# Performance work log

Measured on AMD Instinct MI355X. Metric: run time of the kernel, lower is better.

Reference implementation:

```python
import jax, jax.numpy as jnp
import numpy as np

BN_EPS = 1e-5  # PyTorch BatchNorm1d default eps (Dice's self.eps is unused by its bn)

def _bn(x):
    # training-mode BatchNorm1d without affine: batch mean / biased variance
    m = jnp.mean(x, axis=0)
    v = jnp.var(x, axis=0)
    return (x - m) * jax.lax.rsqrt(v + BN_EPS)

def _dice(x, alpha):
    p = jax.nn.sigmoid(_bn(x))
    return alpha * (1.0 - p) * x + p * x

def setup_inputs():
    key = jax.random.key(0)
    ks = jax.random.split(key, 48)
    B, L = 8192, 200
    Vu, Vd, Va, Vs, Vg, Vt, Vf = 100001, 1001, 50001, 20001, 20001, 501, 100001
    f = jnp.float32
    s = 0.05
    inp = {}
    inp['dense'] = jax.random.normal(ks[0], (B, 16), f)
    inp['userid'] = jax.random.randint(ks[1], (B,), 0, Vu)
    inp['device'] = jax.random.randint(ks[2], (B,), 0, Vd)
    inp['authorid'] = jax.random.randint(ks[3], (B,), 0, Va)
    inp['bgm_song_id'] = jax.random.randint(ks[4], (B,), 0, Vs)
    inp['bgm_singer_id'] = jax.random.randint(ks[5], (B,), 0, Vg)
    inp['manual_tag'] = jax.random.randint(ks[6], (B,), 0, Vt)
    inp['feedid'] = jax.random.randint(ks[7], (B,), 0, Vf)
    inp['seq_ids'] = jax.random.randint(ks[8], (B, L), 0, Vf)
    inp['seq_len'] = jax.random.randint(ks[9], (B,), 1, L + 1)
    # embedding tables (dims hard-coded in the torch module)
    inp['emb_userid'] = s * jax.random.normal(ks[10], (Vu, 16), f)
    inp['emb_device'] = s * jax.random.normal(ks[11], (Vd, 2), f)
    inp['emb_authorid'] = s * jax.random.normal(ks[12], (Va, 4), f)
    inp['emb_song'] = s * jax.random.normal(ks[13], (Vs, 4), f)
    inp['emb_singer'] = s * jax.random.normal(ks[14], (Vg, 4), f)
    inp['emb_tag'] = s * jax.random.normal(ks[15], (Vt, 4), f)
    inp['emb_feedid'] = s * jax.random.normal(ks[16], (Vf, 16), f)
    inp['emb_seq'] = s * jax.random.normal(ks[17], (Vf, 16), f)
    # attention MLP: 4*16 -> 64 -> 32 -> 1
    inp['aW1'] = s * jax.random.normal(ks[18], (64, 64), f)
    inp['ab1'] = jnp.zeros((64,), f)
    inp['aW2'] = s * jax.random.normal(ks[19], (64, 32), f)
    inp['ab2'] = jnp.zeros((32,), f)
    inp['aW3'] = s * jax.random.normal(ks[20], (32, 1), f)
    inp['ab3'] = jnp.zeros((1,), f)
    # FCN stack: 82 -> 512 -> 256 -> 128 -> 1, Dice alpha + affine BN per layer
    dims = [82, 512, 256, 128]
    for i in range(3):
        inp[f'W{i}'] = s * jax.random.normal(ks[21 + i], (dims[i], dims[i + 1]), f)
        inp[f'b{i}'] = jnp.zeros((dims[i + 1],), f)
        inp[f'alpha{i}'] = jnp.zeros((dims[i + 1],), f)
        inp[f'g{i}'] = jnp.ones((dims[i + 1],), f)
        inp[f'beta{i}'] = jnp.zeros((dims[i + 1],), f)
    inp['Wout'] = s * jax.random.normal(ks[30], (128, 1), f)
    inp['bout'] = jnp.zeros((1,), f)
    return inp

def _forward(dense, userid, device, authorid, bgm_song_id, bgm_singer_id, manual_tag,
             feedid, seq_ids, seq_len,
             emb_userid, emb_device, emb_authorid, emb_song, emb_singer, emb_tag,
             emb_feedid, emb_seq,
             aW1, ab1, aW2, ab2, aW3, ab3,
             W0, b0, alpha0, g0, beta0,
             W1, b1, alpha1, g1, beta1,
             W2, b2, alpha2, g2, beta2,
             Wout, bout):
    B, L = seq_ids.shape
    # embedding lookups
    cat_embs = [emb_userid[userid], emb_device[device], emb_authorid[authorid],
                emb_song[bgm_song_id], emb_singer[bgm_singer_id], emb_tag[manual_tag]]
    q = emb_feedid[feedid]            # [B, 16]
    keys = emb_seq[seq_ids]           # [B, L, 16]
    # DIN attention: cross features + 3-layer MLP score
    qe = jnp.broadcast_to(q[:, None, :], keys.shape)
    cross = jnp.concatenate([qe, keys, qe - keys, qe * keys], axis=2)  # [B, L, 64]
    h = jax.nn.relu(cross @ aW1 + ab1)
    h = jax.nn.relu(h @ aW2 + ab2)
    score = (h @ aW3 + ab3)[..., 0]   # [B, L]
    mask = jnp.arange(L)[None, :] < seq_len[:, None]
    w = jnp.where(mask, score, 0.0)   # is_softmax=False branch
    att_out = jnp.sum(w[:, :, None] * keys, axis=1)  # [B, 16]
    # dense MLP stack with Dice + affine BN (dropout is identity at eval)
    net = jnp.concatenate([dense] + cat_embs + [q, att_out], axis=1)  # [B, 82]
    for W, b, a, g, be in ((W0, b0, alpha0, g0, beta0),
                           (W1, b1, alpha1, g1, beta1),
                           (W2, b2, alpha2, g2, beta2)):
        net = net @ W + b
        net = _dice(net, a)
        net = g * _bn(net) + be
    logit = net @ Wout + bout
    prob = jax.nn.sigmoid(logit)
    emb_vars = jnp.concatenate(cat_embs + [q, att_out], axis=1)
    l2_reg = 0.2 * jnp.mean(jnp.linalg.norm(emb_vars, axis=1))
    return prob, logit, l2_reg

def reference(dense, userid, device, authorid, bgm_song_id, bgm_singer_id, manual_tag,
              feedid, seq_ids, seq_len,
              emb_userid, emb_device, emb_authorid, emb_song, emb_singer, emb_tag,
              emb_feedid, emb_seq,
              aW1, ab1, aW2, ab2, aW3, ab3,
              W0, b0, alpha0, g0, beta0,
              W1, b1, alpha1, g1, beta1,
              W2, b2, alpha2, g2, beta2,
              Wout, bout):
    return _forward(dense, userid, device, authorid, bgm_song_id, bgm_singer_id, manual_tag,
                    feedid, seq_ids, seq_len,
                    emb_userid, emb_device, emb_authorid, emb_song, emb_singer, emb_tag,
                    emb_feedid, emb_seq,
                    aW1, ab1, aW2, ab2, aW3, ab3,
                    W0, b0, alpha0, g0, beta0,
                    W1, b1, alpha1, g1, beta1,
                    W2, b2, alpha2, g2, beta2,
                    Wout, bout)
```

## Files before the change

### kernel.cpp

```cpp
#include <hip/hip_runtime.h>
#include <hip/hip_bf16.h>

#define B_ 8192
#define L_ 200

typedef __attribute__((ext_vector_type(4))) short s4v;
typedef __attribute__((ext_vector_type(8))) short s8v;
typedef __attribute__((ext_vector_type(16))) float f32x16;

__device__ __forceinline__ short f2bf(float f) {
    union { float f; unsigned u; } v; v.f = f;
    unsigned r = (v.u + 0x7fffu + ((v.u >> 16) & 1u)) >> 16;
    return (short)r;
}
__device__ __forceinline__ float bf2f(short s) {
    union { unsigned u; float f; } v; v.u = ((unsigned)(unsigned short)s) << 16;
    return v.f;
}
__device__ __forceinline__ unsigned pk2(float a, float b) {
    return ((unsigned)(unsigned short)f2bf(b) << 16) | (unsigned)(unsigned short)f2bf(a);
}

#define OFF_ATT   0
#define OFF_NETBF (OFF_ATT + B_*16)
#define OFF_X     (OFF_NETBF + B_*64)
#define OFF_D0    (OFF_X + B_*512)
#define OFF_D1    (OFF_D0 + B_*256)
#define OFF_D2    (OFF_D1 + B_*128)
#define OFF_ACC   (OFF_D2 + B_*64)
#define OFF_NORM  (OFF_ACC + 12*512)
#define OFF_PREP  (OFF_NORM + 1)
#define OFF_W0T   (OFF_PREP + 4096)
#define OFF_W1T   (OFF_W0T + 32768)
#define OFF_W2T   (OFF_W1T + 65536)
#define OFF_FB1   (OFF_W2T + 16384)
#define OFF_FB2   (OFF_FB1 + 256)

__global__ __launch_bounds__(256) void init_ws(float* acc, float* fb) {
    for (int i = threadIdx.x; i < 12*512 + 1; i += 256) acc[i] = 0.f;
    if (threadIdx.x < 256 + 128) fb[threadIdx.x] = 0.f;
}

__global__ __launch_bounds__(256) void prep_w(
    const float* __restrict__ aW1, const float* __restrict__ aW2,
    const float* __restrict__ W0, float* __restrict__ wsP, short* __restrict__ W0T)
{
    const int t = threadIdx.x;
    if (blockIdx.x == 0) {
        float* W1B = wsP;
        float* W1D = wsP + 1024;
        float* W1AC = wsP + 2048;
        short* W2F = (short*)(wsP + 3072);
        for (int idx = t; idx < 1024; idx += 256) {
            int r = idx & 7, l = (idx >> 3) & 63, mt = idx >> 9;
            int i = ((l >> 5) << 3) + r, j = mt * 32 + (l & 31);
            W1B[idx] = aW1[(16 + i) * 64 + j] - aW1[(32 + i) * 64 + j];
            W1D[idx] = aW1[(48 + i) * 64 + j];
        }
        for (int idx = t; idx < 1024; idx += 256) {
            int i = idx & 15, j = idx >> 4;
            W1AC[idx] = aW1[i * 64 + j] + aW1[(32 + i) * 64 + j];
        }
        for (int idx = t; idx < 2048; idx += 256) {
            int r = idx & 7, l = (idx >> 3) & 63, ks = idx >> 9;
            int j2 = ks * 16 + ((l >> 5) << 3) + r, n2 = l & 31;
            W2F[idx] = f2bf(aW2[j2 * 32 + n2]);
        }
    }
    for (int idx = blockIdx.x * 256 + t; idx < 512 * 128; idx += 32 * 256) {
        int n = idx & 511, k = idx >> 9;
        W0T[n * 128 + k] = (k < 82) ? f2bf(W0[k * 512 + n]) : (short)0;
    }
}

__global__ __launch_bounds__(256) void prep_fold(
    const float* __restrict__ W, const float* __restrict__ bias,
    const float* __restrict__ sD, const float* __restrict__ qD,
    const float* __restrict__ g, const float* __restrict__ be,
    float invB, int K, int N,
    short* __restrict__ WT, float* __restrict__ fb)
{
    __shared__ short tile[64][65];
    __shared__ float sclS[64], sftS[64];
    __shared__ float red[256];
    const int t = threadIdx.x;
    const int bn = blockIdx.x * 64, bk = blockIdx.y * 64;

    if (t < 64) {
        const int k = bk + t;
        float m = sD[k] * invB;
        float v = fmaf(-m, m, qD[k] * invB);
        float sc = g[k] * rsqrtf(v + 1e-5f);
        sclS[t] = sc;
        sftS[t] = be[k] - m * sc;
    }
    __syncthreads();

    const int nn = t & 63, kk0 = (t >> 6) * 16;
    float part = 0.f;
    #pragma unroll
    for (int i = 0; i < 16; ++i) {
        const int kk = kk0 + i;
        float w = W[(size_t)(bk + kk) * N + bn + nn];
        tile[kk][nn] = f2bf(sclS[kk] * w);
        part = fmaf(sftS[kk], w, part);
    }
    red[t] = part;
    __syncthreads();

    {
        const int n = t >> 2, kp = (t & 3) * 16;
        short* dst = &WT[(size_t)(bn + n) * K + bk + kp];
        #pragma unroll
        for (int i = 0; i < 16; ++i) dst[i] = tile[kp + i][n];
    }
    if (t < 64) {
        float s = red[t] + red[t + 64] + red[t + 128] + red[t + 192];
        if (blockIdx.y == 0) s += bias[bn + t];
        atomicAdd(&fb[bn + t], s);
    }
}

__global__ __launch_bounds__(256) void attn_k(
    const int* __restrict__ feedid, const int* __restrict__ seq_ids,
    const int* __restrict__ seq_len,
    const float* __restrict__ e_feed, const float* __restrict__ e_seq,
    const float* __restrict__ ab1, const float* __restrict__ ab2,
    const float* __restrict__ ab3, const float* __restrict__ aW3,
    const float* __restrict__ wsP, float* __restrict__ att)
{
    __shared__ short KL[224 * 20];
    __shared__ float qS[16];
    __shared__ float qtS[64];
    __shared__ float w3S[32], ab2S[32];
    __shared__ float wS[224];
    __shared__ float pS[16 * 16];

    const float* W1B = wsP;
    const float* W1D = wsP + 1024;
    const float* W1AC = wsP + 2048;
    const short* W2F = (const short*)(wsP + 3072);

    const int b = blockIdx.x, t = threadIdx.x;

    if (t < 16) qS[t] = e_feed[(size_t)feedid[b] * 16 + t];
    if (t >= 32 && t < 64) w3S[t - 32] = aW3[t - 32];
    if (t >= 64 && t < 96) ab2S[t - 64] = ab2[t - 64];
    __syncthreads();

    for (int idx = t; idx < 800; idx += 256) {
        int row = idx >> 2, p = idx & 3;
        int sid = seq_ids[(size_t)b * L_ + row];
        const float4 f4 = ((const float4*)(e_seq + (size_t)sid * 16))[p];
        s4v v; v[0] = f2bf(f4.x); v[1] = f2bf(f4.y); v[2] = f2bf(f4.z); v[3] = f2bf(f4.w);
        *(s4v*)&KL[row * 20 + p * 4] = v;
    }
    if (t < 96) {
        s4v z = {0, 0, 0, 0};
        *(s4v*)&KL[(200 + (t >> 2)) * 20 + (t & 3) * 4] = z;
    }
    if (t < 64) {
        float s = ab1[t];
        #pragma unroll
        for (int i = 0; i < 16; ++i) s = fmaf(qS[i], W1AC[t * 16 + i], s);
        qtS[t] = s;
    }
    __syncthreads();

    const int h = (t >> 5) & 1, l31 = t & 31, l63 = t & 63, wv = t >> 6;

    union U8 { s8v s; unsigned u[4]; };

    U8 a1[2];
    #pragma unroll
    for (int mt = 0; mt < 2; ++mt)
        #pragma unroll
        for (int r = 0; r < 8; ++r) {
            int idx = (mt * 64 + l63) * 8 + r;
            float v = fmaf(qS[h * 8 + r], W1D[idx], W1B[idx]);
            a1[mt].s[r] = f2bf(v);
        }
    s8v w2f[4];
    #pragma unroll
    for (int ks = 0; ks < 4; ++ks)
        w2f[ks] = *(const s8v*)&W2F[(ks * 64 + l63) * 8];

    const float ab3v = ab3[0];
    const int len = seq_len[b];

    for (int m = wv; m < 7; m += 4) {
        const int row = m * 32 + l31;
        s8v bK;
        {
            s4v lo = *(const s4v*)&KL[row * 20 + h * 8];
            s4v hi = *(const s4v*)&KL[row * 20 + h * 8 + 4];
            bK[0] = lo[0]; bK[1] = lo[1]; bK[2] = lo[2]; bK[3] = lo[3];
            bK[4] = hi[0]; bK[5] = hi[1]; bK[6] = hi[2]; bK[7] = hi[3];
        }

        f32x16 c2;
        #pragma unroll
        for (int i = 0; i < 16; ++i) c2[i] = 0.f;

        #pragma unroll
        for (int mt = 0; mt < 2; ++mt) {
            f32x16 c;
            #pragma unroll
            for (int i = 0; i < 16; ++i) c[i] = 0.f;
            c = __builtin_amdgcn_mfma_f32_32x32x16_bf16(a1[mt].s, bK, c, 0, 0, 0);

            unsigned pk[8], pks[8];
            #pragma unroll
            for (int i = 0; i < 8; ++i) {
                int r0 = 2 * i, r1 = r0 + 1;
                float v0 = fmaxf(c[r0] + qtS[mt * 32 + (r0 & 3) + 8 * (r0 >> 2) + 4 * h], 0.f);
                float v1 = fmaxf(c[r1] + qtS[mt * 32 + (r1 & 3) + 8 * (r1 >> 2) + 4 * h], 0.f);
                pk[i] = pk2(v0, v1);
                pks[i] = __shfl_xor(pk[i], 32);
            }
            {
                U8 bf2;
                bf2.u[0] = h ? pks[2] : pk[0];
                bf2.u[1] = h ? pks[3] : pk[1];
                bf2.u[2] = h ? pk[2]  : pks[0];
                bf2.u[3] = h ? pk[3]  : pks[1];
                c2 = __builtin_amdgcn_mfma_f32_32x32x16_bf16(w2f[mt * 2], bf2.s, c2, 0, 0, 0);
            }
            {
                U8 bf2;
                bf2.u[0] = h ? pks[6] : pk[4];
                bf2.u[1] = h ? pks[7] : pk[5];
                bf2.u[2] = h ? pk[6]  : pks[4];
                bf2.u[3] = h ? pk[7]  : pks[5];
                c2 = __builtin_amdgcn_mfma_f32_32x32x16_bf16(w2f[mt * 2 + 1], bf2.s, c2, 0, 0, 0);
            }
        }

        float part = 0.f;
        #pragma unroll
        for (int r = 0; r < 16; ++r) {
            int n2 = (r & 3) + 8 * (r >> 2) + 4 * h;
            part = fmaf(fmaxf(c2[r] + ab2S[n2], 0.f), w3S[n2], part);
        }
        float tot = part + __shfl_xor(part, 32) + ab3v;
        if (h == 0) wS[row] = (row < len) ? tot : 0.f;
    }
    __syncthreads();

    {
        const int c = t & 15, ch = t >> 4, r0 = ch * 14;
        float s = 0.f;
        #pragma unroll
        for (int i = 0; i < 14; ++i)
            s = fmaf(wS[r0 + i], bf2f(KL[(r0 + i) * 20 + c]), s);
        pS[ch * 16 + c] = s;
    }
    __syncthreads();
    if (t < 16) {
        float s = 0.f;
        #pragma unroll
        for (int ch = 0; ch < 16; ++ch) s += pS[ch * 16 + t];
        att[(size_t)b * 16 + t] = s;
    }
}

__global__ __launch_bounds__(256) void build_net(
    const float* __restrict__ dense,
    const int* __restrict__ userid, const int* __restrict__ device_,
    const int* __restrict__ authorid, const int* __restrict__ song,
    const int* __restrict__ singer, const int* __restrict__ tag,
    const int* __restrict__ feedid,
    const float* __restrict__ e_user, const float* __restrict__ e_dev,
    const float* __restrict__ e_auth, const float* __restrict__ e_song,
    const float* __restrict__ e_singer, const float* __restrict__ e_tag,
    const float* __restrict__ e_feed,
    const float* __restrict__ att, short* __restrict__ nbf,
    float* __restrict__ norm_acc)
{
    const int b = blockIdx.x * 256 + threadIdx.x;
    float row[82];
    const float* d = dense + (size_t)b * 16;
    #pragma unroll
    for (int i = 0; i < 16; ++i) row[i] = d[i];
    const float* eu = e_user + (size_t)userid[b] * 16;
    #pragma unroll
    for (int i = 0; i < 16; ++i) row[16 + i] = eu[i];
    const float* ed = e_dev + (size_t)device_[b] * 2;
    row[32] = ed[0]; row[33] = ed[1];
    const float* ea = e_auth + (size_t)authorid[b] * 4;
    #pragma unroll
    for (int i = 0; i < 4; ++i) row[34 + i] = ea[i];
    const float* es = e_song + (size_t)song[b] * 4;
    #pragma unroll
    for (int i = 0; i < 4; ++i) row[38 + i] = es[i];
    const float* eg = e_singer + (size_t)singer[b] * 4;
    #pragma unroll
    for (int i = 0; i < 4; ++i) row[42 + i] = eg[i];
    const float* et = e_tag + (size_t)tag[b] * 4;
    #pragma unroll
    for (int i = 0; i < 4; ++i) row[46 + i] = et[i];
    const float* ef = e_feed + (size_t)feedid[b] * 16;
    #pragma unroll
    for (int i = 0; i < 16; ++i) row[50 + i] = ef[i];
    const float* at = att + (size_t)b * 16;
    #pragma unroll
    for (int i = 0; i < 16; ++i) row[66 + i] = at[i];

    float sq = 0.f;
    #pragma unroll
    for (int i = 16; i < 82; ++i) sq = fmaf(row[i], row[i], sq);

    union { unsigned w[64]; uint4 w4[16]; } U;
    #pragma unroll
    for (int i = 0; i < 41; ++i) U.w[i] = pk2(row[2 * i], row[2 * i + 1]);
    #pragma unroll
    for (int i = 41; i < 64; ++i) U.w[i] = 0u;
    uint4* op = (uint4*)(nbf + (size_t)b * 128);
    #pragma unroll
    for (int c = 0; c < 16; ++c) op[c] = U.w4[c];

    float nrm = sqrtf(sq);
    nrm += __shfl_xor(nrm, 32); nrm += __shfl_xor(nrm, 16);
    nrm += __shfl_xor(nrm, 8);  nrm += __shfl_xor(nrm, 4);
    nrm += __shfl_xor(nrm, 2);  nrm += __shfl_xor(nrm, 1);
    if ((threadIdx.x & 63) == 0) atomicAdd(norm_acc, nrm);
}

__global__ __launch_bounds__(256) void gemm_mfma_stats(
    const short* __restrict__ A, int lda,
    const short* __restrict__ BT, int ldb,
    const float* __restrict__ bias,
    float* __restrict__ C, int N, int K,
    float* __restrict__ sout, float* __restrict__ qout)
{
    __shared__ short As[128 * 68];
    __shared__ short Bs[64 * 68];
    __shared__ float colS[64], colQ[64];

    const int bm = blockIdx.y * 128, bn = blockIdx.x * 64;
    const int t = threadIdx.x;
    const int wv = t >> 6, l31 = t & 31, h = (t >> 5) & 1;

    if (t < 64) { colS[t] = 0.f; colQ[t] = 0.f; }

    const int arow0 = t >> 3, apart = (t & 7) * 8;
    s8v ar[4], br[2];

    {   const int k0 = 0;
        #pragma unroll
        for (int i = 0; i < 4; ++i)
            ar[i] = *(const s8v*)&A[(size_t)(bm + arow0 + i * 32) * lda + k0 + apart];
        #pragma unroll
        for (int i = 0; i < 2; ++i)
            br[i] = *(const s8v*)&BT[(size_t)(bn + arow0 + i * 32) * ldb + k0 + apart];
    }

    f32x16 acc0, acc1;
    #pragma unroll
    for (int i = 0; i < 16; ++i) { acc0[i] = 0.f; acc1[i] = 0.f; }

    const int nk = K >> 6;
    for (int kc = 0; kc < nk; ++kc) {
        #pragma unroll
        for (int i = 0; i < 4; ++i)
            *(s8v*)&As[(arow0 + i * 32) * 68 + apart] = ar[i];
        #pragma unroll
        for (int i = 0; i < 2; ++i)
            *(s8v*)&Bs[(arow0 + i * 32) * 68 + apart] = br[i];
        __syncthreads();
        if (kc + 1 < nk) {
            const int k0 = (kc + 1) << 6;
            #pragma unroll
            for (int i = 0; i < 4; ++i)
                ar[i] = *(const s8v*)&A[(size_t)(bm + arow0 + i * 32) * lda + k0 + apart];
            #pragma unroll
            for (int i = 0; i < 2; ++i)
                br[i] = *(const s8v*)&BT[(size_t)(bn + arow0 + i * 32) * ldb + k0 + apart];
        }
        #pragma unroll
        for (int ks = 0; ks < 4; ++ks) {
            const s8v af  = *(const s8v*)&As[(wv * 32 + l31) * 68 + ks * 16 + h * 8];
            const s8v bf0 = *(const s8v*)&Bs[l31 * 68 + ks * 16 + h * 8];
            const s8v bf1 = *(const s8v*)&Bs[(32 + l31) * 68 + ks * 16 + h * 8];
            acc0 = __builtin_amdgcn_mfma_f32_32x32x16_bf16(af, bf0, acc0, 0, 0, 0);
            acc1 = __builtin_amdgcn_mfma_f32_32x32x16_bf16(af, bf1, acc1, 0, 0, 0);
        }
        __syncthreads();
    }

    #pragma unroll
    for (int ns = 0; ns < 2; ++ns) {
        const int col = bn + ns * 32 + l31;
        const float bv = bias[col];
        float s = 0.f, q = 0.f;
        const f32x16& ac = ns ? acc1 : acc0;
        #pragma unroll
        for (int r = 0; r < 16; ++r) {
            const int row = bm + wv * 32 + (r & 3) + 8 * (r >> 2) + 4 * h;
            float x = ac[r] + bv;
            C[(size_t)row * N + col] = x;
            s += x; q = fmaf(x, x, q);
        }
        s += __shfl_xor(s, 32);
        q += __shfl_xor(q, 32);
        if (h == 0) {
            atomicAdd(&colS[ns * 32 + l31], s);
            atomicAdd(&colQ[ns * 32 + l31], q);
        }
    }
    __syncthreads();
    if (t < 64) {
        atomicAdd(&sout[bn + t], colS[t]);
        atomicAdd(&qout[bn + t], colQ[t]);
    }
}

__global__ __launch_bounds__(256) void dice_stats(
    const float* __restrict__ X, short* __restrict__ D,
    const float* __restrict__ sin_, const float* __restrict__ qin_,
    const float* __restrict__ alpha,
    float* __restrict__ sout, float* __restrict__ qout,
    int N, float invB)
{
    __shared__ float cS[64], cQ[64];
    const int t = threadIdx.x;
    const int col = blockIdx.x * 64 + (t & 63);
    const int r0 = blockIdx.y * 64 + (t >> 6);
    if (t < 64) { cS[t] = 0.f; cQ[t] = 0.f; }
    __syncthreads();

    const float m = sin_[col] * invB;
    const float v = fmaf(-m, m, qin_[col] * invB);
    const float rs = rsqrtf(v + 1e-5f);
    const float al = alpha[col];

    float s = 0.f, q = 0.f;
    #pragma unroll
    for (int i = 0; i < 16; ++i) {
        const int r = r0 + i * 4;
        const float x = X[(size_t)r * N + col];
        const float xn = (x - m) * rs;
        const float p = 1.f / (1.f + __expf(-xn));
        const float d = x * (p + al * (1.f - p));
        D[(size_t)r * N + col] = f2bf(d);
        s += d; q = fmaf(d, d, q);
    }
    atomicAdd(&cS[t & 63], s);
    atomicAdd(&cQ[t & 63], q);
    __syncthreads();
    if (t < 64) {
        atomicAdd(&sout[blockIdx.x * 64 + t], cS[t]);
        atomicAdd(&qout[blockIdx.x * 64 + t], cQ[t]);
    }
}

__global__ __launch_bounds__(256) void final_k(
    const short* __restrict__ Y, const float* __restrict__ Wout,
    const float* __restrict__ bout, const float* __restrict__ norm_acc,
    const float* __restrict__ sD, const float* __restrict__ qD,
    const float* __restrict__ g, const float* __restrict__ be,
    float invB, float* __restrict__ out)
{
    const int wv = threadIdx.x >> 6, lane = threadIdx.x & 63;
    const int b = blockIdx.x * 4 + wv;
    const short* y = Y + (size_t)b * 128;

    float s = 0.f;
    #pragma unroll
    for (int hh = 0; hh < 2; ++hh) {
        const int c = hh * 64 + lane;
        const float m = sD[c] * invB;
        const float v = fmaf(-m, m, qD[c] * invB);
        const float yn = g[c] * (bf2f(y[c]) - m) * rsqrtf(v + 1e-5f) + be[c];
        s = fmaf(yn, Wout[c], s);
    }
    s += __shfl_xor(s, 32); s += __shfl_xor(s, 16);
    s += __shfl_xor(s, 8);  s += __shfl_xor(s, 4);
    s += __shfl_xor(s, 2);  s += __shfl_xor(s, 1);
    if (lane == 0) {
        float logit = s + bout[0];
        out[B_ + b] = logit;
        out[b] = 1.f / (1.f + __expf(-logit));
    }
    if (blockIdx.x == 0 && threadIdx.x == 0)
        out[2 * B_] = 0.2f * norm_acc[0] / (float)B_;
}

extern "C" void kernel_launch(void* const* d_in, const int* in_sizes, int n_in,
                              void* d_out, int out_size, void* d_ws, size_t ws_size,
                              hipStream_t stream)
{
    const float* dense    = (const float*)d_in[0];
    const int*   userid   = (const int*)d_in[1];
    const int*   device_  = (const int*)d_in[2];
    const int*   authorid = (const int*)d_in[3];
    const int*   song     = (const int*)d_in[4];
    const int*   singer   = (const int*)d_in[5];
    const int*   tag      = (const int*)d_in[6];
    const int*   feedid   = (const int*)d_in[7];
    const int*   seq_ids  = (const int*)d_in[8];
    const int*   seq_len  = (const int*)d_in[9];
    const float* e_user   = (const float*)d_in[10];
    const float* e_dev    = (const float*)d_in[11];
    const float* e_auth   = (const float*)d_in[12];
    const float* e_song   = (const float*)d_in[13];
    const float* e_singer = (const float*)d_in[14];
    const float* e_tag    = (const float*)d_in[15];
    const float* e_feed   = (const float*)d_in[16];
    const float* e_seq    = (const float*)d_in[17];
    const float* aW1 = (const float*)d_in[18];
    const float* ab1 = (const float*)d_in[19];
    const float* aW2 = (const float*)d_in[20];
    const float* ab2 = (const float*)d_in[21];
    const float* aW3 = (const float*)d_in[22];
    const float* ab3 = (const float*)d_in[23];
    const float* W0 = (const float*)d_in[24]; const float* b0 = (const float*)d_in[25];
    const float* al0 = (const float*)d_in[26]; const float* g0 = (const float*)d_in[27];
    const float* be0 = (const float*)d_in[28];
    const float* W1 = (const float*)d_in[29]; const float* b1 = (const float*)d_in[30];
    const float* al1 = (const float*)d_in[31]; const float* g1 = (const float*)d_in[32];
    const float* be1 = (const float*)d_in[33];
    const float* W2 = (const float*)d_in[34]; const float* b2 = (const float*)d_in[35];
    const float* al2 = (const float*)d_in[36]; const float* g2 = (const float*)d_in[37];
    const float* be2 = (const float*)d_in[38];
    const float* Wout = (const float*)d_in[39]; const float* bout = (const float*)d_in[40];

    float* ws    = (float*)d_ws;
    float* att   = ws + OFF_ATT;
    short* netbf = (short*)(ws + OFF_NETBF);
    float* X     = ws + OFF_X;
    short* d0    = (short*)(ws + OFF_D0);
    short* d1    = (short*)(ws + OFF_D1);
    short* d2    = (short*)(ws + OFF_D2);
    float* acc   = ws + OFF_ACC;
    float* norm  = ws + OFF_NORM;
    float* prep  = ws + OFF_PREP;
    short* W0T   = (short*)(ws + OFF_W0T);
    short* W1T   = (short*)(ws + OFF_W1T);
    short* W2T   = (short*)(ws + OFF_W2T);
    float* fb1   = ws + OFF_FB1;
    float* fb2   = ws + OFF_FB2;
    float* out   = (float*)d_out;

    float* sX0 = acc + 0*512;  float* qX0 = acc + 1*512;
    float* sD0 = acc + 2*512;  float* qD0 = acc + 3*512;
    float* sX1 = acc + 4*512;  float* qX1 = acc + 5*512;
    float* sD1 = acc + 6*512;  float* qD1 = acc + 7*512;
    float* sX2 = acc + 8*512;  float* qX2 = acc + 9*512;
    float* sD2 = acc + 10*512; float* qD2 = acc + 11*512;

    const float invB = 1.f / (float)B_;

    hipLaunchKernelGGL(init_ws, dim3(1), dim3(256), 0, stream, acc, fb1);
    hipLaunchKernelGGL(prep_w, dim3(32), dim3(256), 0, stream, aW1, aW2, W0, prep, W0T);

    hipLaunchKernelGGL(attn_k, dim3(B_), dim3(256), 0, stream,
                       feedid, seq_ids, seq_len, e_feed, e_seq,
                       ab1, ab2, ab3, aW3, prep, att);

    hipLaunchKernelGGL(build_net, dim3(B_/256), dim3(256), 0, stream,
                       dense, userid, device_, authorid, song, singer, tag, feedid,
                       e_user, e_dev, e_auth, e_song, e_singer, e_tag, e_feed,
                       att, netbf, norm);

    hipLaunchKernelGGL(gemm_mfma_stats, dim3(512/64, B_/128), dim3(256), 0, stream,
                       netbf, 128, W0T, 128, b0, X, 512, 128, sX0, qX0);
    hipLaunchKernelGGL(dice_stats, dim3(512/64, B_/64), dim3(256), 0, stream,
                       X, d0, sX0, qX0, al0, sD0, qD0, 512, invB);
    hipLaunchKernelGGL(prep_fold, dim3(256/64, 512/64), dim3(256), 0, stream,
                       W1, b1, sD0, qD0, g0, be0, invB, 512, 256, W1T, fb1);

    hipLaunchKernelGGL(gemm_mfma_stats, dim3(256/64, B_/128), dim3(256), 0, stream,
                       d0, 512, W1T, 512, fb1, X, 256, 512, sX1, qX1);
    hipLaunchKernelGGL(dice_stats, dim3(256/64, B_/64), dim3(256), 0, stream,
                       X, d1, sX1, qX1, al1, sD1, qD1, 256, invB);
    hipLaunchKernelGGL(prep_fold, dim3(128/64, 256/64), dim3(256), 0, stream,
                       W2, b2, sD1, qD1, g1, be1, invB, 256, 128, W2T, fb2);

    hipLaunchKernelGGL(gemm_mfma_stats, dim3(128/64, B_/128), dim3(256), 0, stream,
                       d1, 256, W2T, 256, fb2, X, 128, 256, sX2, qX2);
    hipLaunchKernelGGL(dice_stats, dim3(128/64, B_/64), dim3(256), 0, stream,
                       X, d2, sX2, qX2, al2, sD2, qD2, 128, invB);

    hipLaunchKernelGGL(final_k, dim3(B_/4), dim3(256), 0, stream,
                       d2, Wout, bout, norm, sD2, qD2, g2, be2, invB, out);
}
```

Baseline: 300.9 us.

## Use MFMA for query-dependent attention weights, shrink GEMM tiles, merge init kernel

Several changes at once. The attention kernel no longer builds a per-block query-scaled first-layer weight in registers. It precomputes key*query products in shared memory and issues a second MFMA, with bf16 weight fragments loaded from the prep buffer. The zero-init kernel is folded into prep_w as an extra block, which saves a launch, and float-to-bf16 packing now uses the v_cvt_pk_bf16_f32 instruction. The GEMM tile shrinks from 128x64 to 64x64 with one accumulator per wave, which doubles the grid for more parallelism but gives less reuse per tile.

```diff
diff --git a/kernel.cpp b/kernel.cpp
--- a/kernel.cpp
+++ b/kernel.cpp
@@ -17,8 +17,10 @@
     union { unsigned u; float f; } v; v.u = ((unsigned)(unsigned short)s) << 16;
     return v.f;
 }
-__device__ __forceinline__ unsigned pk2(float a, float b) {
-    return ((unsigned)(unsigned short)f2bf(b) << 16) | (unsigned)(unsigned short)f2bf(a);
+__device__ __forceinline__ unsigned cvtpk(float a, float b) {
+    unsigned r;
+    asm("v_cvt_pk_bf16_f32 %0, %1, %2" : "=v"(r) : "v"(a), "v"(b));
+    return r;
 }
 
 #define OFF_ATT   0
@@ -36,26 +38,22 @@
 #define OFF_FB1   (OFF_W2T + 16384)
 #define OFF_FB2   (OFF_FB1 + 256)
 
-__global__ __launch_bounds__(256) void init_ws(float* acc, float* fb) {
-    for (int i = threadIdx.x; i < 12*512 + 1; i += 256) acc[i] = 0.f;
-    if (threadIdx.x < 256 + 128) fb[threadIdx.x] = 0.f;
-}
-
 __global__ __launch_bounds__(256) void prep_w(
     const float* __restrict__ aW1, const float* __restrict__ aW2,
-    const float* __restrict__ W0, float* __restrict__ wsP, short* __restrict__ W0T)
+    const float* __restrict__ W0, float* __restrict__ wsP, short* __restrict__ W0T,
+    float* __restrict__ acc, float* __restrict__ fb)
 {
     const int t = threadIdx.x;
     if (blockIdx.x == 0) {
-        float* W1B = wsP;
-        float* W1D = wsP + 1024;
-        float* W1AC = wsP + 2048;
-        short* W2F = (short*)(wsP + 3072);
+        short* W1BC = (short*)wsP;
+        short* W1D  = (short*)(wsP + 512);
+        float* W1AC = wsP + 1024;
+        short* W2F  = (short*)(wsP + 2048);
         for (int idx = t; idx < 1024; idx += 256) {
             int r = idx & 7, l = (idx >> 3) & 63, mt = idx >> 9;
             int i = ((l >> 5) << 3) + r, j = mt * 32 + (l & 31);
-            W1B[idx] = aW1[(16 + i) * 64 + j] - aW1[(32 + i) * 64 + j];
-            W1D[idx] = aW1[(48 + i) * 64 + j];
+            W1BC[idx] = f2bf(aW1[(16 + i) * 64 + j] - aW1[(32 + i) * 64 + j]);
+            W1D[idx]  = f2bf(aW1[(48 + i) * 64 + j]);
         }
         for (int idx = t; idx < 1024; idx += 256) {
             int i = idx & 15, j = idx >> 4;
@@ -66,10 +64,14 @@
             int j2 = ks * 16 + ((l >> 5) << 3) + r, n2 = l & 31;
             W2F[idx] = f2bf(aW2[j2 * 32 + n2]);
         }
-    }
-    for (int idx = blockIdx.x * 256 + t; idx < 512 * 128; idx += 32 * 256) {
-        int n = idx & 511, k = idx >> 9;
-        W0T[n * 128 + k] = (k < 82) ? f2bf(W0[k * 512 + n]) : (short)0;
+    } else if (blockIdx.x == 33) {
+        for (int i = t; i < 12 * 512 + 1; i += 256) acc[i] = 0.f;
+        if (t < 256 + 128) fb[t] = 0.f;
+    } else {
+        for (int idx = (blockIdx.x - 1) * 256 + t; idx < 512 * 128; idx += 32 * 256) {
+            int n = idx & 511, k = idx >> 9;
+            W0T[n * 128 + k] = (k < 82) ? f2bf(W0[k * 512 + n]) : (short)0;
+        }
     }
 }
 
@@ -130,34 +132,44 @@
     const float* __restrict__ wsP, float* __restrict__ att)
 {
     __shared__ short KL[224 * 20];
+    __shared__ short KQ[224 * 20];
+    __shared__ int   sidS[224];
     __shared__ float qS[16];
     __shared__ float qtS[64];
     __shared__ float w3S[32], ab2S[32];
     __shared__ float wS[224];
     __shared__ float pS[16 * 16];
 
-    const float* W1B = wsP;
-    const float* W1D = wsP + 1024;
-    const float* W1AC = wsP + 2048;
-    const short* W2F = (const short*)(wsP + 3072);
+    const short* W1BC = (const short*)wsP;
+    const short* W1D  = (const short*)(wsP + 512);
+    const float* W1AC = wsP + 1024;
+    const short* W2F  = (const short*)(wsP + 2048);
 
     const int b = blockIdx.x, t = threadIdx.x;
 
     if (t < 16) qS[t] = e_feed[(size_t)feedid[b] * 16 + t];
     if (t >= 32 && t < 64) w3S[t - 32] = aW3[t - 32];
     if (t >= 64 && t < 96) ab2S[t - 64] = ab2[t - 64];
+    if (t < 200) sidS[t] = seq_ids[(size_t)b * L_ + t];
     __syncthreads();
 
     for (int idx = t; idx < 800; idx += 256) {
-        int row = idx >> 2, p = idx & 3;
-        int sid = seq_ids[(size_t)b * L_ + row];
+        int row = idx >> 2, p = idx & 3, c0 = p * 4;
+        int sid = sidS[row];
         const float4 f4 = ((const float4*)(e_seq + (size_t)sid * 16))[p];
-        s4v v; v[0] = f2bf(f4.x); v[1] = f2bf(f4.y); v[2] = f2bf(f4.z); v[3] = f2bf(f4.w);
-        *(s4v*)&KL[row * 20 + p * 4] = v;
+        uint2 kk, kq;
+        kk.x = cvtpk(f4.x, f4.y);
+        kk.y = cvtpk(f4.z, f4.w);
+        kq.x = cvtpk(f4.x * qS[c0],     f4.y * qS[c0 + 1]);
+        kq.y = cvtpk(f4.z * qS[c0 + 2], f4.w * qS[c0 + 3]);
+        *(uint2*)&KL[row * 20 + c0] = kk;
+        *(uint2*)&KQ[row * 20 + c0] = kq;
     }
     if (t < 96) {
-        s4v z = {0, 0, 0, 0};
-        *(s4v*)&KL[(200 + (t >> 2)) * 20 + (t & 3) * 4] = z;
+        int row = 200 + (t >> 2), c0 = (t & 3) * 4;
+        uint2 z = {0u, 0u};
+        *(uint2*)&KL[row * 20 + c0] = z;
+        *(uint2*)&KQ[row * 20 + c0] = z;
     }
     if (t < 64) {
         float s = ab1[t];
@@ -165,37 +177,37 @@
         for (int i = 0; i < 16; ++i) s = fmaf(qS[i], W1AC[t * 16 + i], s);
         qtS[t] = s;
     }
-    __syncthreads();
 
     const int h = (t >> 5) & 1, l31 = t & 31, l63 = t & 63, wv = t >> 6;
 
-    union U8 { s8v s; unsigned u[4]; };
-
-    U8 a1[2];
-    #pragma unroll
-    for (int mt = 0; mt < 2; ++mt)
-        #pragma unroll
-        for (int r = 0; r < 8; ++r) {
-            int idx = (mt * 64 + l63) * 8 + r;
-            float v = fmaf(qS[h * 8 + r], W1D[idx], W1B[idx]);
-            a1[mt].s[r] = f2bf(v);
-        }
-    s8v w2f[4];
+    s8v w1bcF[2], w1dF[2], w2f[4];
+    #pragma unroll
+    for (int mt = 0; mt < 2; ++mt) {
+        w1bcF[mt] = *(const s8v*)&W1BC[(mt * 64 + l63) * 8];
+        w1dF[mt]  = *(const s8v*)&W1D[(mt * 64 + l63) * 8];
+    }
     #pragma unroll
     for (int ks = 0; ks < 4; ++ks)
         w2f[ks] = *(const s8v*)&W2F[(ks * 64 + l63) * 8];
 
+    __syncthreads();
+
+    union U8 { s8v s; unsigned u[4]; };
     const float ab3v = ab3[0];
     const int len = seq_len[b];
 
     for (int m = wv; m < 7; m += 4) {
         const int row = m * 32 + l31;
-        s8v bK;
+        s8v bK, bKQ;
         {
             s4v lo = *(const s4v*)&KL[row * 20 + h * 8];
             s4v hi = *(const s4v*)&KL[row * 20 + h * 8 + 4];
             bK[0] = lo[0]; bK[1] = lo[1]; bK[2] = lo[2]; bK[3] = lo[3];
             bK[4] = hi[0]; bK[5] = hi[1]; bK[6] = hi[2]; bK[7] = hi[3];
+            s4v lo2 = *(const s4v*)&KQ[row * 20 + h * 8];
+            s4v hi2 = *(const s4v*)&KQ[row * 20 + h * 8 + 4];
+            bKQ[0] = lo2[0]; bKQ[1] = lo2[1]; bKQ[2] = lo2[2]; bKQ[3] = lo2[3];
+            bKQ[4] = hi2[0]; bKQ[5] = hi2[1]; bKQ[6] = hi2[2]; bKQ[7] = hi2[3];
         }
 
         f32x16 c2;
@@ -207,7 +219,8 @@
             f32x16 c;
             #pragma unroll
             for (int i = 0; i < 16; ++i) c[i] = 0.f;
-            c = __builtin_amdgcn_mfma_f32_32x32x16_bf16(a1[mt].s, bK, c, 0, 0, 0);
+            c = __builtin_amdgcn_mfma_f32_32x32x16_bf16(w1bcF[mt], bK,  c, 0, 0, 0);
+            c = __builtin_amdgcn_mfma_f32_32x32x16_bf16(w1dF[mt],  bKQ, c, 0, 0, 0);
 
             unsigned pk[8], pks[8];
             #pragma unroll
@@ -215,7 +228,7 @@
                 int r0 = 2 * i, r1 = r0 + 1;
                 float v0 = fmaxf(c[r0] + qtS[mt * 32 + (r0 & 3) + 8 * (r0 >> 2) + 4 * h], 0.f);
                 float v1 = fmaxf(c[r1] + qtS[mt * 32 + (r1 & 3) + 8 * (r1 >> 2) + 4 * h], 0.f);
-                pk[i] = pk2(v0, v1);
+                pk[i] = cvtpk(v0, v1);
                 pks[i] = __shfl_xor(pk[i], 32);
             }
             {
@@ -312,7 +325,7 @@
 
     union { unsigned w[64]; uint4 w4[16]; } U;
     #pragma unroll
-    for (int i = 0; i < 41; ++i) U.w[i] = pk2(row[2 * i], row[2 * i + 1]);
+    for (int i = 0; i < 41; ++i) U.w[i] = cvtpk(row[2 * i], row[2 * i + 1]);
     #pragma unroll
     for (int i = 41; i < 64; ++i) U.w[i] = 0u;
     uint4* op = (uint4*)(nbf + (size_t)b * 128);
@@ -333,80 +346,69 @@
     float* __restrict__ C, int N, int K,
     float* __restrict__ sout, float* __restrict__ qout)
 {
-    __shared__ short As[128 * 68];
+    __shared__ short As[64 * 68];
     __shared__ short Bs[64 * 68];
     __shared__ float colS[64], colQ[64];
 
-    const int bm = blockIdx.y * 128, bn = blockIdx.x * 64;
+    const int bm = blockIdx.y * 64, bn = blockIdx.x * 64;
     const int t = threadIdx.x;
     const int wv = t >> 6, l31 = t & 31, h = (t >> 5) & 1;
+    const int qr = wv >> 1, qc = wv & 1;
 
     if (t < 64) { colS[t] = 0.f; colQ[t] = 0.f; }
 
-    const int arow0 = t >> 3, apart = (t & 7) * 8;
-    s8v ar[4], br[2];
-
-    {   const int k0 = 0;
-        #pragma unroll
-        for (int i = 0; i < 4; ++i)
-            ar[i] = *(const s8v*)&A[(size_t)(bm + arow0 + i * 32) * lda + k0 + apart];
-        #pragma unroll
-        for (int i = 0; i < 2; ++i)
-            br[i] = *(const s8v*)&BT[(size_t)(bn + arow0 + i * 32) * ldb + k0 + apart];
-    }
-
-    f32x16 acc0, acc1;
-    #pragma unroll
-    for (int i = 0; i < 16; ++i) { acc0[i] = 0.f; acc1[i] = 0.f; }
+    const int row0 = t >> 3, part = (t & 7) * 8;
+    s8v ar[2], br[2];
+    #pragma unroll
+    for (int i = 0; i < 2; ++i) {
+        ar[i] = *(const s8v*)&A[(size_t)(bm + row0 + i * 32) * lda + part];
+        br[i] = *(const s8v*)&BT[(size_t)(bn + row0 + i * 32) * ldb + part];
+    }
+
+    f32x16 acc;
+    #pragma unroll
+    for (int i = 0; i < 16; ++i) acc[i] = 0.f;
 
     const int nk = K >> 6;
     for (int kc = 0; kc < nk; ++kc) {
         #pragma unroll
-        for (int i = 0; i < 4; ++i)
-            *(s8v*)&As[(arow0 + i * 32) * 68 + apart] = ar[i];
-        #pragma unroll
-        for (int i = 0; i < 2; ++i)
-            *(s8v*)&Bs[(arow0 + i * 32) * 68 + apart] = br[i];
+        for (int i = 0; i < 2; ++i) {
+            *(s8v*)&As[(row0 + i * 32) * 68 + part] = ar[i];
+            *(s8v*)&Bs[(row0 + i * 32) * 68 + part] = br[i];
+        }
         __syncthreads();
         if (kc + 1 < nk) {
             const int k0 = (kc + 1) << 6;
             #pragma unroll
-            for (int i = 0; i < 4; ++i)
-                ar[i] = *(const s8v*)&A[(size_t)(bm + arow0 + i * 32) * lda + k0 + apart];
-            #pragma unroll
-            for (int i = 0; i < 2; ++i)
-                br[i] = *(const s8v*)&BT[(size_t)(bn + arow0 + i * 32) * ldb + k0 + apart];
+            for (int i = 0; i < 2; ++i) {
+                ar[i] = *(const s8v*)&A[(size_t)(bm + row0 + i * 32) * lda + k0 + part];
+                br[i] = *(const s8v*)&BT[(size_t)(bn + row0 + i * 32) * ldb + k0 + part];
+            }
         }
         #pragma unroll
         for (int ks = 0; ks < 4; ++ks) {
-            const s8v af  = *(const s8v*)&As[(wv * 32 + l31) * 68 + ks * 16 + h * 8];
-            const s8v bf0 = *(const s8v*)&Bs[l31 * 68 + ks * 16 + h * 8];
-            const s8v bf1 = *(const s8v*)&Bs[(32 + l31) * 68 + ks * 16 + h * 8];
-            acc0 = __builtin_amdgcn_mfma_f32_32x32x16_bf16(af, bf0, acc0, 0, 0, 0);
-            acc1 = __builtin_amdgcn_mfma_f32_32x32x16_bf16(af, bf1, acc1, 0, 0, 0);
+            const s8v af = *(const s8v*)&As[(qr * 32 + l31) * 68 + ks * 16 + h * 8];
+            const s8v bf = *(const s8v*)&Bs[(qc * 32 + l31) * 68 + ks * 16 + h * 8];
+            acc = __builtin_amdgcn_mfma_f32_32x32x16_bf16(af, bf, acc, 0, 0, 0);
         }
         __syncthreads();
     }
 
-    #pragma unroll
-    for (int ns = 0; ns < 2; ++ns) {
-        const int col = bn + ns * 32 + l31;
-        const float bv = bias[col];
-        float s = 0.f, q = 0.f;
-        const f32x16& ac = ns ? acc1 : acc0;
-        #pragma unroll
-        for (int r = 0; r < 16; ++r) {
-            const int row = bm + wv * 32 + (r & 3) + 8 * (r >> 2) + 4 * h;
-            float x = ac[r] + bv;
-            C[(size_t)row * N + col] = x;
-            s += x; q = fmaf(x, x, q);
-        }
-        s += __shfl_xor(s, 32);
-        q += __shfl_xor(q, 32);
-        if (h == 0) {
-            atomicAdd(&colS[ns * 32 + l31], s);
-            atomicAdd(&colQ[ns * 32 + l31], q);
-        }
+    const int col = bn + qc * 32 + l31;
+    const float bv = bias[col];
+    float s = 0.f, q = 0.f;
+    #pragma unroll
+    for (int r = 0; r < 16; ++r) {
+        const int row = bm + qr * 32 + (r & 3) + 8 * (r >> 2) + 4 * h;
+        float x = acc[r] + bv;
+        C[(size_t)row * N + col] = x;
+        s += x; q = fmaf(x, x, q);
+    }
+    s += __shfl_xor(s, 32);
+    q += __shfl_xor(q, 32);
+    if (h == 0) {
+        atomicAdd(&colS[qc * 32 + l31], s);
+        atomicAdd(&colQ[qc * 32 + l31], q);
     }
     __syncthreads();
     if (t < 64) {
@@ -551,8 +553,8 @@
 
     const float invB = 1.f / (float)B_;
 
-    hipLaunchKernelGGL(init_ws, dim3(1), dim3(256), 0, stream, acc, fb1);
-    hipLaunchKernelGGL(prep_w, dim3(32), dim3(256), 0, stream, aW1, aW2, W0, prep, W0T);
+    hipLaunchKernelGGL(prep_w, dim3(34), dim3(256), 0, stream,
+                       aW1, aW2, W0, prep, W0T, acc, fb1);
 
     hipLaunchKernelGGL(attn_k, dim3(B_), dim3(256), 0, stream,
                        feedid, seq_ids, seq_len, e_feed, e_seq,
@@ -563,21 +565,21 @@
                        e_user, e_dev, e_auth, e_song, e_singer, e_tag, e_feed,
                        att, netbf, norm);
 
-    hipLaunchKernelGGL(gemm_mfma_stats, dim3(512/64, B_/128), dim3(256), 0, stream,
+    hipLaunchKernelGGL(gemm_mfma_stats, dim3(512/64, B_/64), dim3(256), 0, stream,
                        netbf, 128, W0T, 128, b0, X, 512, 128, sX0, qX0);
     hipLaunchKernelGGL(dice_stats, dim3(512/64, B_/64), dim3(256), 0, stream,
                        X, d0, sX0, qX0, al0, sD0, qD0, 512, invB);
     hipLaunchKernelGGL(prep_fold, dim3(256/64, 512/64), dim3(256), 0, stream,
                        W1, b1, sD0, qD0, g0, be0, invB, 512, 256, W1T, fb1);
 
-    hipLaunchKernelGGL(gemm_mfma_stats, dim3(256/64, B_/128), dim3(256), 0, stream,
+    hipLaunchKernelGGL(gemm_mfma_stats, dim3(256/64, B_/64), dim3(256), 0, stream,
                        d0, 512, W1T, 512, fb1, X, 256, 512, sX1, qX1);
     hipLaunchKernelGGL(dice_stats, dim3(256/64, B_/64), dim3(256), 0, stream,
                        X, d1, sX1, qX1, al1, sD1, qD1, 256, invB);
     hipLaunchKernelGGL(prep_fold, dim3(128/64, 256/64), dim3(256), 0, stream,
                        W2, b2, sD1, qD1, g1, be1, invB, 256, 128, W2T, fb2);
 
-    hipLaunchKernelGGL(gemm_mfma_stats, dim3(128/64, B_/128), dim3(256), 0, stream,
+    hipLaunchKernelGGL(gemm_mfma_stats, dim3(128/64, B_/64), dim3(256), 0, stream,
                        d1, 256, W2T, 256, fb2, X, 128, 256, sX2, qX2);
     hipLaunchKernelGGL(dice_stats, dim3(128/64, B_/64), dim3(256), 0, stream,
                        X, d2, sX2, qX2, al2, sD2, qD2, 128, invB);
```

Result: faster. 275.9 us (-8.3%).
